# Kernel tuning notes

Measured on AMD Instinct MI355X. Metric: run time of the kernel, lower is better.

The kernel has to match this reference:

```python
import jax, jax.numpy as jnp
import numpy as np
import math

WS = 8      # window_size
SS = 4      # stride = window_size // 2
NHEADS = 4

def _grid(size, ws, ss):
    n = (size - ws) // ss + 1
    return jnp.arange(n)[:, None] * ss + jnp.arange(ws)[None, :]  # (n, ws)

def _unfold(x, ws, ss):
    # x: (B,C,Hp,Wp) -> (B, L, C, ws*ws), matching torch F.unfold ordering
    B, C, Hp, Wp = x.shape
    ri = _grid(Hp, ws, ss)
    ci = _grid(Wp, ws, ss)
    p = x[:, :, ri][:, :, :, :, ci]  # (B,C,nH,ws,nW,ws)
    nH, nW = ri.shape[0], ci.shape[0]
    p = p.transpose(0, 2, 4, 1, 3, 5).reshape(B, nH * nW, C, ws * ws)
    return p, nH, nW

def _fold(p, Hp, Wp, nH, nW, ws, ss):
    # p: (B, L, C, ws*ws) -> overlap-add to (B,C,Hp,Wp), matching torch F.fold
    B, L, C, _ = p.shape
    p = p.reshape(B, nH, nW, C, ws, ws).transpose(0, 3, 1, 4, 2, 5)  # (B,C,nH,ws,nW,ws)
    rr = _grid(Hp, ws, ss)[:, :, None, None]   # (nH,ws,1,1)
    cc = _grid(Wp, ws, ss)[None, None, :, :]   # (1,1,nW,ws)
    return jnp.zeros((B, C, Hp, Wp), p.dtype).at[:, :, rr, cc].add(p)

def _se(h, w1, w2):
    # squeeze-excite: global avg pool -> 1x1 reduce -> relu -> 1x1 expand -> sigmoid gate
    pooled = h.mean(axis=(2, 3))                                # (B, gc)
    s = jax.nn.sigmoid(jax.nn.relu(pooled @ w1.T) @ w2.T)       # (B, gc)
    return h * s[:, :, None, None]

def _forward(low, high, w_ql, w_kh, w_vh, w_qh, w_kl, w_vl, w_proj_l, w_proj_h,
             se0_w1, se0_w2, se1_w1, se1_w2, se2_w1, se2_w2):
    B, C, H, W = low.shape
    ws, ss = WS, SS
    n_h = 0 if H <= ws else math.ceil((H - ws) / ss)
    n_w = 0 if W <= ws else math.ceil((W - ws) / ss)
    Hp, Wp = n_h * ss + ws, n_w * ss + ws
    pad = ((0, 0), (0, 0), (0, Hp - H), (0, Wp - W))
    low_p = jnp.pad(low, pad)
    high_p = jnp.pad(high, pad)
    base, rem = divmod(C, 3)
    chs = [base + (1 if i < rem else 0) for i in range(3)]
    ofs = np.cumsum([0] + chs)
    sew = [(se0_w1, se0_w2), (se1_w1, se1_w2), (se2_w1, se2_w2)]
    high_dir = jnp.concatenate(
        [_se(high_p[:, ofs[i]:ofs[i + 1]], *sew[i]) for i in range(3)], axis=1)
    lw, nH, nW = _unfold(low_p, ws, ss)    # (B,L,C,Np)
    hw, _, _ = _unfold(high_dir, ws, ss)
    L, Np, d = lw.shape[1], ws * ws, C // NHEADS
    scale = d ** -0.5
    proj = lambda x, w: jnp.einsum('oc,blcn->blon', w, x).reshape(B, L, NHEADS, d, Np)
    a_lh = jax.nn.softmax(jnp.einsum('blhdn,blhdm->blhnm', proj(lw, w_ql), proj(hw, w_kh)) * scale, axis=-1)
    a_hl = jax.nn.softmax(jnp.einsum('blhdn,blhdm->blhnm', proj(hw, w_qh), proj(lw, w_kl)) * scale, axis=-1)
    ol = jnp.einsum('blhnm,blhdm->blhdn', a_lh, proj(hw, w_vh)).reshape(B, L, C, Np)
    oh = jnp.einsum('blhnm,blhdm->blhdn', a_hl, proj(lw, w_vl)).reshape(B, L, C, Np)
    mask = _fold(jnp.ones((1, L, 1, Np), low.dtype), Hp, Wp, nH, nW, ws, ss)  # overlap counts
    out_l = (_fold(ol, Hp, Wp, nH, nW, ws, ss) / mask)[:, :, :H, :W]
    out_h = (_fold(oh, Hp, Wp, nH, nW, ws, ss) / mask)[:, :, :H, :W]
    return (low + jnp.einsum('oc,bchw->bohw', w_proj_l, out_l),
            high + jnp.einsum('oc,bchw->bohw', w_proj_h, out_h))

def setup_inputs() -> dict:
    key = jax.random.key(0)
    ks = jax.random.split(key, 20)
    B, C, H, W = 4, 64, 128, 128
    chs = [22, 21, 21]
    d = {
        'low': jax.random.normal(ks[0], (B, C, H, W), jnp.float32),
        'high': jax.random.normal(ks[1], (B, C, H, W), jnp.float32),
    }
    for i, n in enumerate(['w_ql', 'w_kh', 'w_vh', 'w_qh', 'w_kl', 'w_vl', 'w_proj_l', 'w_proj_h']):
        d[n] = jax.random.normal(ks[2 + i], (C, C), jnp.float32) * (C ** -0.5)
    for i, gc in enumerate(chs):
        d[f'se{i}_w1'] = jax.random.normal(ks[10 + 2 * i], (1, gc), jnp.float32) * 0.1
        d[f'se{i}_w2'] = jax.random.normal(ks[11 + 2 * i], (gc, 1), jnp.float32) * 0.1
    return d

def reference(low, high, w_ql, w_kh, w_vh, w_qh, w_kl, w_vl, w_proj_l, w_proj_h,
              se0_w1, se0_w2, se1_w1, se1_w2, se2_w1, se2_w2):
    return _forward(low, high, w_ql, w_kh, w_vh, w_qh, w_kl, w_vl, w_proj_l, w_proj_h,
                    se0_w1, se0_w2, se1_w1, se1_w2, se2_w1, se2_w2)
```

## Files before the change

kernel.cpp:

```cpp
#include <hip/hip_runtime.h>

typedef short short8 __attribute__((ext_vector_type(8)));
typedef short short4v __attribute__((ext_vector_type(4)));
typedef float f4 __attribute__((ext_vector_type(4)));

#define NB 4
#define NHW 128
#define NPX (NHW*NHW)
#define NWIN 31
#define NL (NWIN*NWIN)
#define SWV(r,c) (((r)<<6) + (((((c)>>3) ^ ((r)&7))<<3) | ((c)&7)))
#define MFMA(a,b,c) __builtin_amdgcn_mfma_f32_16x16x32_bf16(a,b,c,0,0,0)

__device__ __forceinline__ short f2bf(float f) {
    unsigned u = __float_as_uint(f);
    u += 0x7fffu + ((u >> 16) & 1u);
    return (short)(u >> 16);
}
__device__ __forceinline__ short f2bft(float f) {
    return (short)(__float_as_uint(f) >> 16);
}
__device__ __forceinline__ float bf2f(short v) {
    return __uint_as_float(((unsigned)(unsigned short)v) << 16);
}

__global__ void k_pool(const float* __restrict__ high, float* __restrict__ pooled) {
    int bc = blockIdx.x;
    const float* src = high + (size_t)bc * NPX;
    float s = 0.f;
    for (int i = threadIdx.x; i < NPX; i += 256) s += src[i];
    for (int off = 32; off > 0; off >>= 1) s += __shfl_down(s, off);
    __shared__ float red[4];
    int lane = threadIdx.x & 63, wv = threadIdx.x >> 6;
    if (lane == 0) red[wv] = s;
    __syncthreads();
    if (threadIdx.x == 0)
        pooled[bc] = (red[0] + red[1] + red[2] + red[3]) * (1.f / NPX);
}

__global__ void k_gate(const float* __restrict__ pooled,
                       const float* __restrict__ w10, const float* __restrict__ w20,
                       const float* __restrict__ w11, const float* __restrict__ w21,
                       const float* __restrict__ w12, const float* __restrict__ w22,
                       float* __restrict__ sgate) {
    __shared__ float pl[256];
    int t = threadIdx.x;
    pl[t] = pooled[t];
    __syncthreads();
    int b = t >> 6, c = t & 63;
    const float* w1; const float* w2; int o0, gc;
    if (c < 22)      { w1 = w10; w2 = w20; o0 = 0;  gc = 22; }
    else if (c < 43) { w1 = w11; w2 = w21; o0 = 22; gc = 21; }
    else             { w1 = w12; w2 = w22; o0 = 43; gc = 21; }
    float a = 0.f;
    for (int k = 0; k < gc; ++k) a += pl[b*64 + o0 + k] * w1[k];
    a = fmaxf(a, 0.f);
    float z = a * w2[c - o0];
    sgate[t] = 1.f / (1.f + __expf(-z));
}

__device__ __forceinline__ void wrange(int x, int& lo, int& hi) {
    lo = (x >= 7) ? ((x - 4) >> 2) : 0;
    hi = x >> 2; if (hi > 30) hi = 30;
}

template<int EMIT>
__device__ __forceinline__ void proj_body(
    const float* __restrict__ src, const float* __restrict__ gate,
    const float* __restrict__ Wq, const float* __restrict__ Wk, const float* __restrict__ Wv,
    short* __restrict__ Qp, short* __restrict__ Kp, short* __restrict__ Vp,
    short* T, int b, int row, int t) {
    const float* sp = src + (size_t)b*64*NPX + row*NHW;
    #pragma unroll
    for (int i = 0; i < 8; ++i) {
        int f = t + i*256;
        int c = f & 63, px = (f >> 6) << 2;
        float4 v = *(const float4*)(sp + (size_t)c*NPX + px);
        float g = gate ? gate[b*64 + c] : 1.f;
        T[SWV(px + 0, c)] = f2bf(v.x * g);
        T[SWV(px + 1, c)] = f2bf(v.y * g);
        T[SWV(px + 2, c)] = f2bf(v.z * g);
        T[SWV(px + 3, c)] = f2bf(v.w * g);
    }
    __syncthreads();
    int w = t >> 6, ln = t & 63, l16 = ln & 15, quad = ln >> 4;
    int orow = 16*w + l16;
    short8 wq[2], wk[2], wv[2];
    #pragma unroll
    for (int kf = 0; kf < 2; ++kf) {
        if (EMIT & 1) {
            const float* p = Wq + orow*64 + kf*32 + quad*8;
            #pragma unroll
            for (int j = 0; j < 8; ++j) wq[kf][j] = f2bf(p[j]);
        }
        if (EMIT & 2) {
            const float* p = Wk + orow*64 + kf*32 + quad*8;
            #pragma unroll
            for (int j = 0; j < 8; ++j) wk[kf][j] = f2bf(p[j]);
        }
        if (EMIT & 4) {
            const float* p = Wv + orow*64 + kf*32 + quad*8;
            #pragma unroll
            for (int j = 0; j < 8; ++j) wv[kf][j] = f2bf(p[j]);
        }
    }
    #pragma unroll
    for (int nt = 0; nt < 8; ++nt) {
        int px = nt*16 + l16;
        short8 xb0 = *(const short8*)(T + SWV(px, quad*8));
        short8 xb1 = *(const short8*)(T + SWV(px, 32 + quad*8));
        size_t clbase = ((size_t)b*NPX + row*NHW + px)*64 + 16*w + quad*4;
        if (EMIT & 1) {
            f4 acc = {0.f,0.f,0.f,0.f};
            acc = MFMA(wq[0], xb0, acc); acc = MFMA(wq[1], xb1, acc);
            short4v sv;
            #pragma unroll
            for (int r = 0; r < 4; ++r) sv[r] = f2bf(acc[r] * 0.25f);
            *(short4v*)(Qp + clbase) = sv;
        }
        if (EMIT & 2) {
            f4 acc = {0.f,0.f,0.f,0.f};
            acc = MFMA(wk[0], xb0, acc); acc = MFMA(wk[1], xb1, acc);
            short4v sv;
            #pragma unroll
            for (int r = 0; r < 4; ++r) sv[r] = f2bf(acc[r]);
            *(short4v*)(Kp + clbase) = sv;
        }
        if (EMIT & 4) {
            f4 acc = {0.f,0.f,0.f,0.f};
            acc = MFMA(wv[0], xb0, acc); acc = MFMA(wv[1], xb1, acc);
            #pragma unroll
            for (int r = 0; r < 4; ++r)
                Vp[((size_t)(b*64 + 16*w + quad*4 + r))*NPX + row*NHW + px] = f2bf(acc[r]);
        }
    }
}

template<int EMIT>
__global__ __launch_bounds__(256, 6) void k_proj(
    const float* __restrict__ src, const float* __restrict__ gate,
    const float* __restrict__ Wq, const float* __restrict__ Wk, const float* __restrict__ Wv,
    short* __restrict__ Qp, short* __restrict__ Kp, short* __restrict__ Vp) {
    __shared__ __align__(16) short T[8192];
    proj_body<EMIT>(src, gate, Wq, Wk, Wv, Qp, Kp, Vp, T,
                    blockIdx.x >> 7, blockIdx.x & 127, threadIdx.x);
}

__global__ __launch_bounds__(256, 6) void k_proj2(
    const float* __restrict__ s0, const float* __restrict__ s1, const float* __restrict__ gate,
    const float* __restrict__ Wq0, const float* __restrict__ Wk0, const float* __restrict__ Wv0,
    const float* __restrict__ Wq1, const float* __restrict__ Wk1, const float* __restrict__ Wv1,
    short* __restrict__ Q0, short* __restrict__ K0, short* __restrict__ V0,
    short* __restrict__ Q1, short* __restrict__ K1, short* __restrict__ V1) {
    __shared__ __align__(16) short T[8192];
    int region = blockIdx.x & 7;
    int ss = region >> 2, b = region & 3, row = blockIdx.x >> 3;
    if (ss == 0)
        proj_body<7>(s0, nullptr, Wq0, Wk0, Wv0, Q0, K0, V0, T, b, row, threadIdx.x);
    else
        proj_body<7>(s1, gate, Wq1, Wk1, Wv1, Q1, K1, V1, T, b, row, threadIdx.x);
}

template<int SWZ>
__global__ __launch_bounds__(256, 6) void k_attn(
    const short* __restrict__ Q0, const short* __restrict__ K0, const short* __restrict__ V0,
    const short* __restrict__ Q1, const short* __restrict__ K1, const short* __restrict__ V1,
    short* __restrict__ scr, size_t scr_stride, int nb) {
    __shared__ __align__(16) short Pb[4][1024];
    int bidx = blockIdx.x;
    int pass, b, l;
    if (SWZ) {
        int region = bidx & 7;
        pass = region >> 2; b = region & 3; l = bidx >> 3;
    } else {
        int per = nb * NL;
        pass = bidx / per; int rem2 = bidx - pass*per;
        b = rem2 / NL; l = rem2 - b*NL;
    }
    const short* Qp = pass ? Q1 : Q0;
    const short* Kp = pass ? K1 : K0;
    const short* Vp = pass ? V1 : V0;
    short* scrp = scr + (size_t)pass * scr_stride;
    int wr = l / NWIN, wc = l - (l/NWIN)*NWIN;
    int row0 = wr*4, col0 = wc*4;
    int parity = (wr & 1)*2 + (wc & 1);
    int t = threadIdx.x, w = t >> 6, ln = t & 63, l16 = ln & 15, quad = ln >> 4;
    int h = w;
    short* PT = Pb[w];
    short8 z = {0,0,0,0,0,0,0,0};
    const short one = (short)0x3F80;
    short8 ones = {one,one,one,one,one,one,one,one};

    short8 kb[4];
    #pragma unroll
    for (int mt = 0; mt < 4; ++mt) {
        int m = mt*16 + l16;
        int px = (row0 + (m >> 3))*NHW + col0 + (m & 7);
        kb[mt] = (quad < 2) ? *(const short8*)(Kp + ((size_t)b*NPX + px)*64 + h*16 + quad*8) : z;
    }
    short8 va0, va1;
    {
        const short* vb = Vp + ((size_t)(b*64 + h*16 + l16))*NPX;
        const short* p0 = vb + (row0 + quad)*NHW + col0;
        const short* p1 = vb + (row0 + 4 + quad)*NHW + col0;
        short4v a = *(const short4v*)p0, bq = *(const short4v*)(p0 + 4);
        short4v c = *(const short4v*)p1, d = *(const short4v*)(p1 + 4);
        #pragma unroll
        for (int j = 0; j < 4; ++j) { va0[j] = a[j]; va0[4+j] = bq[j]; va1[j] = c[j]; va1[4+j] = d[j]; }
    }

    #pragma unroll
    for (int ntl = 0; ntl < 4; ++ntl) {
        int n = ntl*16 + l16;
        int px = (row0 + (n >> 3))*NHW + col0 + (n & 7);
        short8 qa = (quad < 2) ? *(const short8*)(Qp + ((size_t)b*NPX + px)*64 + h*16 + quad*8) : z;
        f4 s[4];
        #pragma unroll
        for (int mt = 0; mt < 4; ++mt) {
            f4 acc = {0.f,0.f,0.f,0.f};
            s[mt] = MFMA(qa, kb[mt], acc);
        }
        #pragma unroll
        for (int mt = 0; mt < 4; ++mt)
            #pragma unroll
            for (int r = 0; r < 4; ++r)
                PT[SWV(quad*4 + r, mt*16 + l16)] = f2bft(__expf(fminf(s[mt][r], 30.f)));
        short8 pb0 = *(const short8*)(PT + SWV(l16, quad*8));
        short8 pb1 = *(const short8*)(PT + SWV(l16, 32 + quad*8));
        f4 o = {0.f,0.f,0.f,0.f};
        o = MFMA(va0, pb0, o);
        o = MFMA(va1, pb1, o);
        f4 dn = {0.f,0.f,0.f,0.f};
        dn = MFMA(ones, pb0, dn);
        dn = MFMA(ones, pb1, dn);
        float inv = __builtin_amdgcn_rcpf(dn[0]);
        short4v sv;
        #pragma unroll
        for (int r = 0; r < 4; ++r) sv[r] = f2bf(o[r] * inv);
        *(short4v*)(scrp + (((size_t)(parity*nb + b))*NPX + px)*64 + h*16 + quad*4) = sv;
    }
}

template<int SWZ>
__global__ __launch_bounds__(256, 6) void k_gather(
    const short* __restrict__ scr, size_t scr_stride,
    const float* __restrict__ r0, const float* __restrict__ r1,
    const float* __restrict__ wp0, const float* __restrict__ wp1,
    float* __restrict__ o0, float* __restrict__ o1, int nb) {
    __shared__ __align__(16) short G[4096];
    int bidx = blockIdx.x;
    int pass, b, hh, half;
    if (SWZ) {
        int region = bidx & 7;
        pass = region >> 2; b = region & 3;
        int rem2 = bidx >> 3; hh = rem2 >> 1; half = rem2 & 1;
    } else {
        pass = 0;
        b = bidx / (NHW*2); int rem2 = bidx - b*(NHW*2);
        hh = rem2 >> 1; half = rem2 & 1;
    }
    const short* scrp = scr + (size_t)pass * scr_stride;
    const float* resid = pass ? r1 : r0;
    const float* wproj = pass ? wp1 : wp0;
    float* outp = pass ? o1 : o0;
    int t = threadIdx.x;
    int ploc = t >> 2, c0 = (t & 3)*16;
    int p = half*64 + ploc;
    int rlo, rhi, clo, chi;
    wrange(hh, rlo, rhi); wrange(p, clo, chi);
    float vr[2], vc[2];
    vr[0] = (rhi > rlo || (rlo & 1) == 0) ? 1.f : 0.f;
    vr[1] = (rhi > rlo || (rlo & 1) == 1) ? 1.f : 0.f;
    vc[0] = (chi > clo || (clo & 1) == 0) ? 1.f : 0.f;
    vc[1] = (chi > clo || (clo & 1) == 1) ? 1.f : 0.f;
    float g[16];
    #pragma unroll
    for (int k = 0; k < 16; ++k) g[k] = 0.f;
    #pragma unroll
    for (int par = 0; par < 4; ++par) {
        float wgt = vr[par >> 1] * vc[par & 1];
        const short* srcp = scrp + (((size_t)(par*nb + b))*NPX + hh*NHW + p)*64 + c0;
        #pragma unroll
        for (int k8 = 0; k8 < 2; ++k8) {
            short8 v = *(const short8*)(srcp + k8*8);
            #pragma unroll
            for (int j = 0; j < 8; ++j) g[k8*8 + j] += wgt * bf2f(v[j]);
        }
    }
    float inv = 1.f / ((float)(rhi - rlo + 1) * (float)(chi - clo + 1));
    #pragma unroll
    for (int k8 = 0; k8 < 2; ++k8) {
        short8 v;
        #pragma unroll
        for (int j = 0; j < 8; ++j) v[j] = f2bf(g[k8*8 + j] * inv);
        *(short8*)(G + SWV(ploc, c0 + k8*8)) = v;
    }
    __syncthreads();
    int w = t >> 6, ln = t & 63, l16 = ln & 15, quad = ln >> 4;
    short8 wa0, wa1;
    {
        const float* p0 = wproj + (16*w + l16)*64 + quad*8;
        #pragma unroll
        for (int j = 0; j < 8; ++j) { wa0[j] = f2bf(p0[j]); wa1[j] = f2bf(p0[32 + j]); }
    }
    #pragma unroll
    for (int pt = 0; pt < 4; ++pt) {
        f4 acc = {0.f,0.f,0.f,0.f};
        acc = MFMA(wa0, *(const short8*)(G + SWV(pt*16 + l16, quad*8)), acc);
        acc = MFMA(wa1, *(const short8*)(G + SWV(pt*16 + l16, 32 + quad*8)), acc);
        #pragma unroll
        for (int r = 0; r < 4; ++r) {
            size_t gi = (((size_t)(b*64 + 16*w + quad*4 + r))*NHW + hh)*NHW + half*64 + pt*16 + l16;
            outp[gi] = resid[gi] + acc[r];
        }
    }
}

extern "C" void kernel_launch(void* const* d_in, const int* in_sizes, int n_in,
                              void* d_out, int out_size, void* d_ws, size_t ws_size,
                              hipStream_t stream) {
    const float* low  = (const float*)d_in[0];
    const float* high = (const float*)d_in[1];
    const float* w_ql = (const float*)d_in[2];
    const float* w_kh = (const float*)d_in[3];
    const float* w_vh = (const float*)d_in[4];
    const float* w_qh = (const float*)d_in[5];
    const float* w_kl = (const float*)d_in[6];
    const float* w_vl = (const float*)d_in[7];
    const float* w_pl = (const float*)d_in[8];
    const float* w_ph = (const float*)d_in[9];
    float* out = (float*)d_out;
    float* pooled = (float*)d_ws;
    float* sgate  = pooled + 256;
    short* base = (short*)((char*)d_ws + 2048);
    const size_t PL = (size_t)NB * NPX * 64;
    const size_t plane_f = (size_t)NB * 64 * NPX;
    const size_t SCR = 4 * PL;
    size_t need_fused  = 2048 + (6*PL + 2*SCR) * sizeof(short);
    size_t need_serial = 2048 + (6*PL + SCR) * sizeof(short);
    size_t scr_elems_per_b = 4 * (size_t)NPX * 64;

    k_pool<<<dim3(NB*64), dim3(256), 0, stream>>>(high, pooled);
    k_gate<<<dim3(1), dim3(256), 0, stream>>>(pooled,
        (const float*)d_in[10], (const float*)d_in[11],
        (const float*)d_in[12], (const float*)d_in[13],
        (const float*)d_in[14], (const float*)d_in[15], sgate);

    if (ws_size >= need_serial) {
        short* QL = base;        short* KL = base + PL;   short* VL = base + 2*PL;
        short* QH = base + 3*PL; short* KH = base + 4*PL; short* VH = base + 5*PL;
        short* scr = base + 6*PL;
        k_proj2<<<dim3(8*NHW), dim3(256), 0, stream>>>(low, high, sgate,
            w_ql, w_kl, w_vl, w_qh, w_kh, w_vh,
            QL, KL, VL, QH, KH, VH);
        if (ws_size >= need_fused) {
            k_attn<1><<<dim3(8*NL), dim3(256), 0, stream>>>(QL, KH, VH, QH, KL, VL, scr, SCR, NB);
            k_gather<1><<<dim3(8*NHW*2), dim3(256), 0, stream>>>(scr, SCR, low, high,
                w_pl, w_ph, out, out + plane_f, NB);
        } else {
            k_attn<0><<<dim3(NB*NL), dim3(256), 0, stream>>>(QL, KH, VH, nullptr, nullptr, nullptr, scr, 0, NB);
            k_gather<0><<<dim3(NB*NHW*2), dim3(256), 0, stream>>>(scr, 0, low, nullptr,
                w_pl, nullptr, out, nullptr, NB);
            k_attn<0><<<dim3(NB*NL), dim3(256), 0, stream>>>(QH, KL, VL, nullptr, nullptr, nullptr, scr, 0, NB);
            k_gather<0><<<dim3(NB*NHW*2), dim3(256), 0, stream>>>(scr, 0, high, nullptr,
                w_ph, nullptr, out + plane_f, nullptr, NB);
        }
    } else {
        short* P0 = base; short* P1 = base + PL; short* P2 = base + 2*PL;
        short* scr = base + 3*PL;
        int nbc = 0;
        for (int n = NB; n >= 1; n >>= 1)
            if (ws_size >= 2048 + (3*PL + n*scr_elems_per_b)*sizeof(short)) { nbc = n; break; }
        if (nbc == 0) nbc = 1;
        for (int pass = 0; pass < 2; ++pass) {
            const float* qsrc = pass ? high : low;
            const float* ksrc = pass ? low  : high;
            const float* qg   = pass ? sgate : nullptr;
            const float* kg   = pass ? nullptr : sgate;
            const float* Wq   = pass ? w_qh : w_ql;
            const float* Wk   = pass ? w_kl : w_kh;
            const float* Wv   = pass ? w_vl : w_vh;
            const float* Wp   = pass ? w_ph : w_pl;
            const float* resid = pass ? high : low;
            float* op = out + (size_t)pass * plane_f;
            k_proj<1><<<dim3(NB*NHW), dim3(256), 0, stream>>>(qsrc, qg, Wq, nullptr, nullptr, P0, nullptr, nullptr);
            k_proj<6><<<dim3(NB*NHW), dim3(256), 0, stream>>>(ksrc, kg, nullptr, Wk, Wv, nullptr, P1, P2);
            for (int b0 = 0; b0 < NB; b0 += nbc) {
                int nb = (NB - b0) < nbc ? (NB - b0) : nbc;
                size_t boff = (size_t)b0 * NPX * 64;
                k_attn<0><<<dim3(nb*NL), dim3(256), 0, stream>>>(P0 + boff, P1 + boff, P2 + boff,
                    nullptr, nullptr, nullptr, scr, 0, nb);
                k_gather<0><<<dim3(nb*NHW*2), dim3(256), 0, stream>>>(scr, 0, resid + boff, nullptr,
                    Wp, nullptr, op + boff, nullptr, nb);
            }
        }
    }
}
```

Measured before the change: 218.3 us.

## Fold parity sum into MFMA projection and pre-convert proj weights to bf16

The gather kernel no longer sums the four parity scratch planes in fp32, rounds to bf16 and stages them in LDS before projecting. It now feeds each parity plane straight into MFMAs against the projection weights, accumulates across parities, and applies the window-count normalisation after the matmul. The bf16 conversion of the projection weights moves into the gate kernel so gather loads ready bf16 fragments. This removes the LDS staging and barrier but runs four times more MFMAs, keeps more weight registers live, and lowers the launch-bounds occupancy hint from 6 to 4.

```diff
diff --git a/kernel.cpp b/kernel.cpp
--- a/kernel.cpp
+++ b/kernel.cpp
@@ -42,10 +42,17 @@
                        const float* __restrict__ w10, const float* __restrict__ w20,
                        const float* __restrict__ w11, const float* __restrict__ w21,
                        const float* __restrict__ w12, const float* __restrict__ w22,
-                       float* __restrict__ sgate) {
+                       const float* __restrict__ wpl, const float* __restrict__ wph,
+                       float* __restrict__ sgate, short* __restrict__ wbf) {
     __shared__ float pl[256];
     int t = threadIdx.x;
     pl[t] = pooled[t];
+    #pragma unroll
+    for (int i = 0; i < 32; ++i) {
+        int idx = t + i*256;
+        const float* src = (idx < 4096) ? wpl : wph;
+        wbf[idx] = f2bf(src[idx & 4095]);
+    }
     __syncthreads();
     int b = t >> 6, c = t & 63;
     const float* w1; const float* w2; int o0, gc;
@@ -242,12 +249,11 @@
 }
 
 template<int SWZ>
-__global__ __launch_bounds__(256, 6) void k_gather(
+__global__ __launch_bounds__(256, 4) void k_gather(
     const short* __restrict__ scr, size_t scr_stride,
     const float* __restrict__ r0, const float* __restrict__ r1,
-    const float* __restrict__ wp0, const float* __restrict__ wp1,
+    const short* __restrict__ wpb,
     float* __restrict__ o0, float* __restrict__ o1, int nb) {
-    __shared__ __align__(16) short G[4096];
     int bidx = blockIdx.x;
     int pass, b, hh, half;
     if (SWZ) {
@@ -261,59 +267,47 @@
     }
     const short* scrp = scr + (size_t)pass * scr_stride;
     const float* resid = pass ? r1 : r0;
-    const float* wproj = pass ? wp1 : wp0;
+    const short* wproj = wpb + (SWZ ? pass*4096 : 0);
     float* outp = pass ? o1 : o0;
-    int t = threadIdx.x;
-    int ploc = t >> 2, c0 = (t & 3)*16;
-    int p = half*64 + ploc;
+    int t = threadIdx.x, w = t >> 6, ln = t & 63, l16 = ln & 15, quad = ln >> 4;
+    int px = half*64 + w*16 + l16;
     int rlo, rhi, clo, chi;
-    wrange(hh, rlo, rhi); wrange(p, clo, chi);
-    float vr[2], vc[2];
-    vr[0] = (rhi > rlo || (rlo & 1) == 0) ? 1.f : 0.f;
-    vr[1] = (rhi > rlo || (rlo & 1) == 1) ? 1.f : 0.f;
-    vc[0] = (chi > clo || (clo & 1) == 0) ? 1.f : 0.f;
-    vc[1] = (chi > clo || (clo & 1) == 1) ? 1.f : 0.f;
-    float g[16];
-    #pragma unroll
-    for (int k = 0; k < 16; ++k) g[k] = 0.f;
+    wrange(hh, rlo, rhi); wrange(px, clo, chi);
+    bool okr0 = (rhi > rlo) || ((rlo & 1) == 0);
+    bool okr1 = (rhi > rlo) || ((rlo & 1) == 1);
+    bool okc0 = (chi > clo) || ((clo & 1) == 0);
+    bool okc1 = (chi > clo) || ((clo & 1) == 1);
+    short8 wa[4][2];
+    #pragma unroll
+    for (int ct = 0; ct < 4; ++ct)
+        #pragma unroll
+        for (int kf = 0; kf < 2; ++kf)
+            wa[ct][kf] = *(const short8*)(wproj + (ct*16 + l16)*64 + kf*32 + quad*8);
+    f4 acc[4];
+    #pragma unroll
+    for (int ct = 0; ct < 4; ++ct) acc[ct] = (f4){0.f,0.f,0.f,0.f};
+    short8 z = {0,0,0,0,0,0,0,0};
     #pragma unroll
     for (int par = 0; par < 4; ++par) {
-        float wgt = vr[par >> 1] * vc[par & 1];
-        const short* srcp = scrp + (((size_t)(par*nb + b))*NPX + hh*NHW + p)*64 + c0;
-        #pragma unroll
-        for (int k8 = 0; k8 < 2; ++k8) {
-            short8 v = *(const short8*)(srcp + k8*8);
-            #pragma unroll
-            for (int j = 0; j < 8; ++j) g[k8*8 + j] += wgt * bf2f(v[j]);
+        bool valid = ((par >> 1) ? okr1 : okr0) && ((par & 1) ? okc1 : okc0);
+        const short* sp2 = scrp + (((size_t)(par*nb + b))*NPX + hh*NHW + px)*64;
+        short8 b0 = *(const short8*)(sp2 + quad*8);
+        short8 b1 = *(const short8*)(sp2 + 32 + quad*8);
+        if (!valid) { b0 = z; b1 = z; }
+        #pragma unroll
+        for (int ct = 0; ct < 4; ++ct) {
+            acc[ct] = MFMA(wa[ct][0], b0, acc[ct]);
+            acc[ct] = MFMA(wa[ct][1], b1, acc[ct]);
         }
     }
     float inv = 1.f / ((float)(rhi - rlo + 1) * (float)(chi - clo + 1));
     #pragma unroll
-    for (int k8 = 0; k8 < 2; ++k8) {
-        short8 v;
-        #pragma unroll
-        for (int j = 0; j < 8; ++j) v[j] = f2bf(g[k8*8 + j] * inv);
-        *(short8*)(G + SWV(ploc, c0 + k8*8)) = v;
-    }
-    __syncthreads();
-    int w = t >> 6, ln = t & 63, l16 = ln & 15, quad = ln >> 4;
-    short8 wa0, wa1;
-    {
-        const float* p0 = wproj + (16*w + l16)*64 + quad*8;
-        #pragma unroll
-        for (int j = 0; j < 8; ++j) { wa0[j] = f2bf(p0[j]); wa1[j] = f2bf(p0[32 + j]); }
-    }
-    #pragma unroll
-    for (int pt = 0; pt < 4; ++pt) {
-        f4 acc = {0.f,0.f,0.f,0.f};
-        acc = MFMA(wa0, *(const short8*)(G + SWV(pt*16 + l16, quad*8)), acc);
-        acc = MFMA(wa1, *(const short8*)(G + SWV(pt*16 + l16, 32 + quad*8)), acc);
+    for (int ct = 0; ct < 4; ++ct)
         #pragma unroll
         for (int r = 0; r < 4; ++r) {
-            size_t gi = (((size_t)(b*64 + 16*w + quad*4 + r))*NHW + hh)*NHW + half*64 + pt*16 + l16;
-            outp[gi] = resid[gi] + acc[r];
-        }
-    }
+            size_t gi = (((size_t)(b*64 + ct*16 + quad*4 + r))*NHW + hh)*NHW + px;
+            outp[gi] = resid[gi] + acc[ct][r] * inv;
+        }
 }
 
 extern "C" void kernel_launch(void* const* d_in, const int* in_sizes, int n_in,
@@ -332,19 +326,22 @@
     float* out = (float*)d_out;
     float* pooled = (float*)d_ws;
     float* sgate  = pooled + 256;
-    short* base = (short*)((char*)d_ws + 2048);
+    short* wbf = (short*)((char*)d_ws + 2048);
+    short* base = wbf + 8192;
     const size_t PL = (size_t)NB * NPX * 64;
     const size_t plane_f = (size_t)NB * 64 * NPX;
     const size_t SCR = 4 * PL;
-    size_t need_fused  = 2048 + (6*PL + 2*SCR) * sizeof(short);
-    size_t need_serial = 2048 + (6*PL + SCR) * sizeof(short);
+    const size_t HDR = 2048 + 8192*sizeof(short);
+    size_t need_fused  = HDR + (6*PL + 2*SCR) * sizeof(short);
+    size_t need_serial = HDR + (6*PL + SCR) * sizeof(short);
     size_t scr_elems_per_b = 4 * (size_t)NPX * 64;
 
     k_pool<<<dim3(NB*64), dim3(256), 0, stream>>>(high, pooled);
     k_gate<<<dim3(1), dim3(256), 0, stream>>>(pooled,
         (const float*)d_in[10], (const float*)d_in[11],
         (const float*)d_in[12], (const float*)d_in[13],
-        (const float*)d_in[14], (const float*)d_in[15], sgate);
+        (const float*)d_in[14], (const float*)d_in[15],
+        w_pl, w_ph, sgate, wbf);
 
     if (ws_size >= need_serial) {
         short* QL = base;        short* KL = base + PL;   short* VL = base + 2*PL;
@@ -356,21 +353,21 @@
         if (ws_size >= need_fused) {
             k_attn<1><<<dim3(8*NL), dim3(256), 0, stream>>>(QL, KH, VH, QH, KL, VL, scr, SCR, NB);
             k_gather<1><<<dim3(8*NHW*2), dim3(256), 0, stream>>>(scr, SCR, low, high,
-                w_pl, w_ph, out, out + plane_f, NB);
+                wbf, out, out + plane_f, NB);
         } else {
             k_attn<0><<<dim3(NB*NL), dim3(256), 0, stream>>>(QL, KH, VH, nullptr, nullptr, nullptr, scr, 0, NB);
             k_gather<0><<<dim3(NB*NHW*2), dim3(256), 0, stream>>>(scr, 0, low, nullptr,
-                w_pl, nullptr, out, nullptr, NB);
+                wbf, out, nullptr, NB);
             k_attn<0><<<dim3(NB*NL), dim3(256), 0, stream>>>(QH, KL, VL, nullptr, nullptr, nullptr, scr, 0, NB);
             k_gather<0><<<dim3(NB*NHW*2), dim3(256), 0, stream>>>(scr, 0, high, nullptr,
-                w_ph, nullptr, out + plane_f, nullptr, NB);
+                wbf + 4096, out + plane_f, nullptr, NB);
         }
     } else {
         short* P0 = base; short* P1 = base + PL; short* P2 = base + 2*PL;
         short* scr = base + 3*PL;
         int nbc = 0;
         for (int n = NB; n >= 1; n >>= 1)
-            if (ws_size >= 2048 + (3*PL + n*scr_elems_per_b)*sizeof(short)) { nbc = n; break; }
+            if (ws_size >= HDR + (3*PL + n*scr_elems_per_b)*sizeof(short)) { nbc = n; break; }
         if (nbc == 0) nbc = 1;
         for (int pass = 0; pass < 2; ++pass) {
             const float* qsrc = pass ? high : low;
@@ -380,7 +377,7 @@
             const float* Wq   = pass ? w_qh : w_ql;
             const float* Wk   = pass ? w_kl : w_kh;
             const float* Wv   = pass ? w_vl : w_vh;
-            const float* Wp   = pass ? w_ph : w_pl;
+            const short* Wpb  = wbf + pass*4096;
             const float* resid = pass ? high : low;
             float* op = out + (size_t)pass * plane_f;
             k_proj<1><<<dim3(NB*NHW), dim3(256), 0, stream>>>(qsrc, qg, Wq, nullptr, nullptr, P0, nullptr, nullptr);
@@ -391,7 +388,7 @@
                 k_attn<0><<<dim3(nb*NL), dim3(256), 0, stream>>>(P0 + boff, P1 + boff, P2 + boff,
                     nullptr, nullptr, nullptr, scr, 0, nb);
                 k_gather<0><<<dim3(nb*NHW*2), dim3(256), 0, stream>>>(scr, 0, resid + boff, nullptr,
-                    Wp, nullptr, op + boff, nullptr, nb);
+                    Wpb, op + boff, nullptr, nb);
             }
         }
     }
```

New measurement: 224.0 us. 1.03x slower.
